# Optimization experiments

Hardware: AMD Instinct MI355X
Metric: run time of the kernel (lower is better)

Reference implementation:

```python
import jax, jax.numpy as jnp
import numpy as np

SIGMA_V = 0.1   # std of topic-level Gaussian noise theta_V
SCALE_R = 0.1   # 'sigma2_R' is used as the Normal scale in the torch code


def setup_inputs() -> dict:
    key = jax.random.key(0)
    ks = jax.random.split(key, 8)
    T, L, NT, KC, D = 20, 2000, 1000, 256, 5
    return {
        "Q": jax.random.normal(ks[0], (NT, 32), dtype=jnp.float32),
        "V": jax.random.normal(ks[1], (NT, KC), dtype=jnp.float32),
        "R": jax.random.uniform(ks[2], (T, L, NT), dtype=jnp.float32),
        "neighbor_weights": jax.random.normal(ks[3], (NT, NT), dtype=jnp.float32),
        "U": jax.random.normal(ks[4], (T, L, KC, D), dtype=jnp.float32),
        "U_emb_w": jax.random.normal(ks[5], (1, D), dtype=jnp.float32),
        "U_emb_b": jax.random.normal(ks[6], (1,), dtype=jnp.float32),
        "noise": jax.random.normal(ks[7], (NT, KC), dtype=jnp.float32),
        "C": jax.random.randint(jax.random.fold_in(key, 9), (T, L, NT), 0, 2, dtype=jnp.int32),
    }


def reference(Q, V, R, neighbor_weights, U, U_emb_w, U_emb_b, noise, C):
    # (nw[:, :, None] * V[None]).sum(0)[b, k] == V[b, k] * nw.sum(0)[b]
    # -> avoid materializing the (nt, nt, kc) intermediate.
    V_j = V * jnp.sum(neighbor_weights, axis=0)[:, None] + SIGMA_V * noise  # (nt, kc)
    # Linear(dim=5 -> 1) applied to U, then squeeze: (T, L, kc)
    U_emb = jnp.einsum('tlkd,d->tlk', U, U_emb_w[0]) + U_emb_b[0]
    # scores[t, i, j] = sigmoid(U_emb[t, i, :] . V_j[j, :])
    mu = jax.nn.sigmoid(jnp.einsum('tlk,jk->tlj', U_emb, V_j))  # (T, L, nt)
    # Normal(mu, SCALE_R).log_prob(R), summed over entries where C == 1
    log_prob = (-0.5 * jnp.square((R - mu) / SCALE_R)
                - jnp.log(SCALE_R) - 0.5 * jnp.log(2.0 * jnp.pi))
    return jnp.sum(jnp.where(C == 1, log_prob, 0.0))
```

## Files before the change

### kernel.cpp

```cpp
#include <hip/hip_runtime.h>
#include <hip/hip_bf16.h>

typedef __attribute__((ext_vector_type(8))) short short8;
typedef __attribute__((ext_vector_type(4))) float f32x4;
typedef __attribute__((ext_vector_type(4))) int   i32x4;

#define NTOP 1000
#define KC   256
#define MROWS 40000
#define MBLK  64

static __device__ __forceinline__ unsigned short f2bf(float x) {
    union { float f; unsigned u; } v; v.f = x;
    unsigned r = (v.u + 0x7FFFu + ((v.u >> 16) & 1u)) >> 16;
    return (unsigned short)r;
}

__global__ void k_prep(const float* __restrict__ nw,
                       float* __restrict__ colsum) {
    int j  = blockIdx.x * 256 + threadIdx.x;
    int i0 = blockIdx.y * 8;
    if (j < NTOP) {
        float s = 0.f;
        int iend = min(i0 + 8, NTOP);
        for (int i = i0; i < iend; ++i) s += nw[(size_t)i * NTOP + j];
        atomicAdd(colsum + j, s);
    }
}

__global__ void k_vj(const float* __restrict__ V,
                     const float* __restrict__ noise,
                     const float* __restrict__ colsum,
                     unsigned short* __restrict__ Bp) {
    int t  = blockIdx.x * 256 + threadIdx.x;
    int nt = t >> 9;
    int s  = (t >> 6) & 7;
    int l  = t & 63;
    int lm = l & 15, lq = l >> 4;
    int n  = nt * 16 + lm;
    int k0 = s * 32 + lq * 8;
    union { short8 v; unsigned short us[8]; } pk;
    if (n < NTOP) {
        float cs = colsum[n];
        #pragma unroll
        for (int j = 0; j < 8; ++j) {
            int idx = n * KC + k0 + j;
            pk.us[j] = f2bf(V[idx] * cs + 0.1f * noise[idx]);
        }
    } else {
        #pragma unroll
        for (int j = 0; j < 8; ++j) pk.us[j] = 0;
    }
    reinterpret_cast<short8*>(Bp)[t] = pk.v;
}

__global__ __launch_bounds__(256) void k_cmask(const int* __restrict__ C,
                                               unsigned* __restrict__ Cb) {
    const int idx = blockIdx.x * 256 + threadIdx.x;
    const int m = idx >> 5, w = idx & 31;
    const int* p = C + (size_t)m * NTOP + w * 32;
    const int nbase = w * 32;
    unsigned word = 0;
    if (nbase + 32 <= NTOP) {
        #pragma unroll
        for (int j = 0; j < 32; j += 4) {
            i32x4 c4 = *reinterpret_cast<const i32x4*>(p + j);
            word |= (unsigned)(c4.x == 1) << (j + 0);
            word |= (unsigned)(c4.y == 1) << (j + 1);
            word |= (unsigned)(c4.z == 1) << (j + 2);
            word |= (unsigned)(c4.w == 1) << (j + 3);
        }
    } else {
        for (int j = 0; j < NTOP - nbase; ++j)
            word |= (unsigned)(p[j] == 1) << j;
    }
    Cb[idx] = word;
}


#define SBAR __builtin_amdgcn_sched_barrier(0)

#define LOADBF8(nt_, B0,B1,B2,B3,B4,B5,B6,B7) do {                        \
    const short8* bp_ = Bf + ((((nt_) * 8) << 6) + l);                    \
    B0 = bp_[0*64]; B1 = bp_[1*64]; B2 = bp_[2*64]; B3 = bp_[3*64];       \
    B4 = bp_[4*64]; B5 = bp_[5*64]; B6 = bp_[6*64]; B7 = bp_[7*64];       \
} while (0)

#define LOADIT8(nt_, R0,R1,R2,R3, W0,W1,W2,W3) do {                       \
    const int nst_ = ((nt_) << 4) + (lq << 2);                            \
    if (nst_ < NTOP) {                                                    \
        const int ws_ = nst_ >> 5;                                        \
        R0 = *reinterpret_cast<const f32x4*>(R + rb0 + nst_);             \
        R1 = *reinterpret_cast<const f32x4*>(R + rb1 + nst_);             \
        R2 = *reinterpret_cast<const f32x4*>(R + rb2 + nst_);             \
        R3 = *reinterpret_cast<const f32x4*>(R + rb3 + nst_);             \
        W0 = Cb[cb0 + ws_]; W1 = Cb[cb1 + ws_];                           \
        W2 = Cb[cb2 + ws_]; W3 = Cb[cb3 + ws_];                           \
    } else {                                                              \
        R0 = (f32x4){0.f,0.f,0.f,0.f}; R1 = (f32x4){0.f,0.f,0.f,0.f};     \
        R2 = (f32x4){0.f,0.f,0.f,0.f}; R3 = (f32x4){0.f,0.f,0.f,0.f};     \
        W0 = 0u; W1 = 0u; W2 = 0u; W3 = 0u;                               \
    }                                                                     \
} while (0)

#define MF1(s_, B_) do {                                                  \
    const short8 a0_ = Afrag[0][s_][l];                                   \
    const short8 a1_ = Afrag[1][s_][l];                                   \
    const short8 a2_ = Afrag[2][s_][l];                                   \
    const short8 a3_ = Afrag[3][s_][l];                                   \
    acc0 = __builtin_amdgcn_mfma_f32_16x16x32_bf16(B_, a0_, acc0, 0,0,0); \
    acc1 = __builtin_amdgcn_mfma_f32_16x16x32_bf16(B_, a1_, acc1, 0,0,0); \
    acc2 = __builtin_amdgcn_mfma_f32_16x16x32_bf16(B_, a2_, acc2, 0,0,0); \
    acc3 = __builtin_amdgcn_mfma_f32_16x16x32_bf16(B_, a3_, acc3, 0,0,0); \
} while (0)

#define MFMA8(B0,B1,B2,B3,B4,B5,B6,B7) do {                               \
    acc0 = (f32x4){0.f,0.f,0.f,0.f}; acc1 = (f32x4){0.f,0.f,0.f,0.f};     \
    acc2 = (f32x4){0.f,0.f,0.f,0.f}; acc3 = (f32x4){0.f,0.f,0.f,0.f};     \
    MF1(0,B0); MF1(1,B1); MF1(2,B2); MF1(3,B3);                           \
    MF1(4,B4); MF1(5,B5); MF1(6,B6); MF1(7,B7);                           \
} while (0)

#define EPI1(ACC, RV, W_, SH) do {                                        \
    const unsigned y_ = (W_) >> (SH);                                     \
    _Pragma("unroll")                                                     \
    for (int r_ = 0; r_ < 4; ++r_) {                                      \
        float muv_ = 1.f / (1.f + __expf(-ACC[r_]));                      \
        float d_   = RV[r_] - muv_;                                       \
        float lp_  = -50.f * d_ * d_ + 1.3836465597893728f;               \
        if ((y_ >> r_) & 1u) lpsum += lp_;                                \
    }                                                                     \
} while (0)

#define EPI8(R0,R1,R2,R3, W0,W1,W2,W3, SH) do {                           \
    EPI1(acc0, R0, W0, SH); EPI1(acc1, R1, W1, SH);                       \
    EPI1(acc2, R2, W2, SH); EPI1(acc3, R3, W3, SH);                       \
} while (0)

__global__ __launch_bounds__(256, 2) void k_main(
    const float* __restrict__ U, const float* __restrict__ w5,
    const float* __restrict__ b1, const short8* __restrict__ Bf,
    const float* __restrict__ R, const unsigned* __restrict__ Cb,
    float* __restrict__ out)
{
    __shared__ short8 Afrag[4][8][64];
    __shared__ float  rawU[5120];

    const int tid  = threadIdx.x;
    const int wave = tid >> 6;
    const int l    = tid & 63;
    const int lm = l & 15;
    const int lq = l >> 4;
    const int m0 = blockIdx.x * MBLK;

    const float w0 = w5[0], w1 = w5[1], w2 = w5[2], w3 = w5[3], w4 = w5[4];
    const float bb = b1[0];

    const float* ub = U + (size_t)m0 * (KC * 5);
    for (int g = 0; g < 16; ++g) {
        const float* src = ub + (size_t)g * 5120;
        #pragma unroll
        for (int j = 0; j < 5; ++j) {
            const int idx = j * 1024 + tid * 4;
            *reinterpret_cast<f32x4*>(&rawU[idx]) =
                *reinterpret_cast<const f32x4*>(src + idx);
        }
        __syncthreads();
        if (tid < 128) {
            const int s   = tid >> 4;
            const int lqc = (tid >> 2) & 3;
            const int lmh = tid & 3;
            const int fi  = lmh * 1280 + s * 160 + lqc * 40;
            float u[40];
            #pragma unroll
            for (int i = 0; i < 10; ++i) {
                f32x4 t = *reinterpret_cast<const f32x4*>(&rawU[fi + i * 4]);
                u[i*4+0] = t.x; u[i*4+1] = t.y; u[i*4+2] = t.z; u[i*4+3] = t.w;
            }
            union { short8 v; unsigned short us[8]; } pk;
            #pragma unroll
            for (int j = 0; j < 8; ++j) {
                float e = u[j*5+0]*w0 + u[j*5+1]*w1 + u[j*5+2]*w2
                        + u[j*5+3]*w3 + u[j*5+4]*w4 + bb;
                pk.us[j] = f2bf(e);
            }
            const int mt = g >> 2;
            const int ll = lqc * 16 + ((g & 3) * 4 + lmh);
            Afrag[mt][s][ll] = pk.v;
        }
        __syncthreads();
    }

    const size_t rb0 = (size_t)(m0 +  0 + lm) * NTOP;
    const size_t rb1 = (size_t)(m0 + 16 + lm) * NTOP;
    const size_t rb2 = (size_t)(m0 + 32 + lm) * NTOP;
    const size_t rb3 = (size_t)(m0 + 48 + lm) * NTOP;
    const size_t cb0 = (size_t)(m0 +  0 + lm) * 32;
    const size_t cb1 = (size_t)(m0 + 16 + lm) * 32;
    const size_t cb2 = (size_t)(m0 + 32 + lm) * 32;
    const size_t cb3 = (size_t)(m0 + 48 + lm) * 32;

    float lpsum = 0.f;
    const int nt0 = wave << 4;
    const int shE = lq << 2;
    const int shO = 16 + (lq << 2);

    short8 pA0, pA1, pA2, pA3, pA4, pA5, pA6, pA7;
    short8 pB0, pB1, pB2, pB3, pB4, pB5, pB6, pB7;
    f32x4  rA0, rA1, rA2, rA3,  rB0, rB1, rB2, rB3;
    unsigned wA0, wA1, wA2, wA3,  wB0, wB1, wB2, wB3;
    f32x4  acc0, acc1, acc2, acc3;

    LOADBF8(nt0, pA0,pA1,pA2,pA3,pA4,pA5,pA6,pA7);
    LOADIT8(nt0, rA0,rA1,rA2,rA3, wA0,wA1,wA2,wA3);

    for (int it2 = 0; it2 < 8; ++it2) {
        const int ntE = nt0 + it2 * 2;

        SBAR;
        LOADBF8(ntE + 1, pB0,pB1,pB2,pB3,pB4,pB5,pB6,pB7);
        SBAR;
        MFMA8(pA0,pA1,pA2,pA3,pA4,pA5,pA6,pA7);
        SBAR;
        LOADIT8(ntE + 1, rB0,rB1,rB2,rB3, wB0,wB1,wB2,wB3);
        SBAR;
        EPI8(rA0,rA1,rA2,rA3, wA0,wA1,wA2,wA3, shE);

        SBAR;
        if (it2 < 7) { LOADBF8(ntE + 2, pA0,pA1,pA2,pA3,pA4,pA5,pA6,pA7); }
        SBAR;
        MFMA8(pB0,pB1,pB2,pB3,pB4,pB5,pB6,pB7);
        SBAR;
        if (it2 < 7) { LOADIT8(ntE + 2, rA0,rA1,rA2,rA3, wA0,wA1,wA2,wA3); }
        SBAR;
        EPI8(rB0,rB1,rB2,rB3, wB0,wB1,wB2,wB3, shO);
    }

    #pragma unroll
    for (int off = 32; off > 0; off >>= 1) lpsum += __shfl_down(lpsum, off);
    if (l == 0) atomicAdd(out, lpsum);
}

extern "C" void kernel_launch(void* const* d_in, const int* in_sizes, int n_in,
                              void* d_out, int out_size, void* d_ws, size_t ws_size,
                              hipStream_t stream) {
    const float* V     = (const float*)d_in[1];
    const float* R     = (const float*)d_in[2];
    const float* nw    = (const float*)d_in[3];
    const float* U     = (const float*)d_in[4];
    const float* w5    = (const float*)d_in[5];
    const float* b1    = (const float*)d_in[6];
    const float* noise = (const float*)d_in[7];
    const int*   C     = (const int*)d_in[8];
    float* out = (float*)d_out;

    float*          colsum = (float*)d_ws;
    unsigned short* Bp     = (unsigned short*)((char*)d_ws + 8192);
    unsigned*       Cb     = (unsigned*)((char*)d_ws + 532480);

    hipMemsetAsync(colsum, 0, NTOP * sizeof(float), stream);
    hipMemsetAsync(out, 0, sizeof(float), stream);
    hipLaunchKernelGGL(k_prep, dim3(4, 125), dim3(256), 0, stream, nw, colsum);
    hipLaunchKernelGGL(k_vj, dim3(128), dim3(256), 0, stream,
                       V, noise, colsum, Bp);
    hipLaunchKernelGGL(k_cmask, dim3(5000), dim3(256), 0, stream, C, Cb);
    hipLaunchKernelGGL(k_main, dim3(MROWS / MBLK), dim3(256), 0, stream,
                       U, w5, b1, (const short8*)Bp, R, Cb, out);
}
```

Baseline: 187.4 us.

## Prefetch U tiles in registers, pad LDS, and deepen main-loop prefetch

The U staging loop now keeps the next U chunk in registers while the current one is converted. The LDS rows are padded to 1284 floats to reduce bank conflicts. All 256 threads now share the bf16 embedding conversion, each doing half a fragment, where only 128 did before. The main loop prefetches two tiles ahead (A and B both loaded before the loop), and launch bounds ask for 3 blocks per SM. This adds register pressure, which may cause spills under the higher occupancy target.

```diff
diff --git a/kernel.cpp b/kernel.cpp
--- a/kernel.cpp
+++ b/kernel.cpp
@@ -4,6 +4,7 @@
 typedef __attribute__((ext_vector_type(8))) short short8;
 typedef __attribute__((ext_vector_type(4))) float f32x4;
 typedef __attribute__((ext_vector_type(4))) int   i32x4;
+typedef __attribute__((ext_vector_type(4))) unsigned short us4;
 
 #define NTOP 1000
 #define KC   256
@@ -137,14 +138,14 @@
     EPI1(acc2, R2, W2, SH); EPI1(acc3, R3, W3, SH);                       \
 } while (0)
 
-__global__ __launch_bounds__(256, 2) void k_main(
+__global__ __launch_bounds__(256, 3) void k_main(
     const float* __restrict__ U, const float* __restrict__ w5,
     const float* __restrict__ b1, const short8* __restrict__ Bf,
     const float* __restrict__ R, const unsigned* __restrict__ Cb,
     float* __restrict__ out)
 {
     __shared__ short8 Afrag[4][8][64];
-    __shared__ float  rawU[5120];
+    __shared__ float  rawU[4 * 1284];
 
     const int tid  = threadIdx.x;
     const int wave = tid >> 6;
@@ -156,39 +157,69 @@
     const float w0 = w5[0], w1 = w5[1], w2 = w5[2], w3 = w5[3], w4 = w5[4];
     const float bb = b1[0];
 
-    const float* ub = U + (size_t)m0 * (KC * 5);
-    for (int g = 0; g < 16; ++g) {
-        const float* src = ub + (size_t)g * 5120;
-        #pragma unroll
-        for (int j = 0; j < 5; ++j) {
-            const int idx = j * 1024 + tid * 4;
-            *reinterpret_cast<f32x4*>(&rawU[idx]) =
-                *reinterpret_cast<const f32x4*>(src + idx);
+    {
+        const float* ub = U + (size_t)m0 * (KC * 5);
+
+        float* dst0; float* dst1; float* dst2; float* dst3; float* dst4;
+        {
+            int i0 = 0 * 1024 + tid * 4; dst0 = &rawU[(i0 / 1280) * 1284 + i0 % 1280];
+            int i1 = 1 * 1024 + tid * 4; dst1 = &rawU[(i1 / 1280) * 1284 + i1 % 1280];
+            int i2 = 2 * 1024 + tid * 4; dst2 = &rawU[(i2 / 1280) * 1284 + i2 % 1280];
+            int i3 = 3 * 1024 + tid * 4; dst3 = &rawU[(i3 / 1280) * 1284 + i3 % 1280];
+            int i4 = 4 * 1024 + tid * 4; dst4 = &rawU[(i4 / 1280) * 1284 + i4 % 1280];
         }
-        __syncthreads();
-        if (tid < 128) {
-            const int s   = tid >> 4;
-            const int lqc = (tid >> 2) & 3;
-            const int lmh = tid & 3;
-            const int fi  = lmh * 1280 + s * 160 + lqc * 40;
-            float u[40];
-            #pragma unroll
-            for (int i = 0; i < 10; ++i) {
-                f32x4 t = *reinterpret_cast<const f32x4*>(&rawU[fi + i * 4]);
-                u[i*4+0] = t.x; u[i*4+1] = t.y; u[i*4+2] = t.z; u[i*4+3] = t.w;
+        const int chunk = tid >> 1;
+        const int half  = tid & 1;
+        const int s_c   = chunk >> 4;
+        const int lqc   = (chunk >> 2) & 3;
+        const int lmh   = chunk & 3;
+        const int fi    = lmh * 1284 + s_c * 160 + lqc * 40 + half * 20;
+
+        f32x4 st0, st1, st2, st3, st4;
+        st0 = *reinterpret_cast<const f32x4*>(ub + 0 * 1024 + tid * 4);
+        st1 = *reinterpret_cast<const f32x4*>(ub + 1 * 1024 + tid * 4);
+        st2 = *reinterpret_cast<const f32x4*>(ub + 2 * 1024 + tid * 4);
+        st3 = *reinterpret_cast<const f32x4*>(ub + 3 * 1024 + tid * 4);
+        st4 = *reinterpret_cast<const f32x4*>(ub + 4 * 1024 + tid * 4);
+
+        for (int g = 0; g < 16; ++g) {
+            *reinterpret_cast<f32x4*>(dst0) = st0;
+            *reinterpret_cast<f32x4*>(dst1) = st1;
+            *reinterpret_cast<f32x4*>(dst2) = st2;
+            *reinterpret_cast<f32x4*>(dst3) = st3;
+            *reinterpret_cast<f32x4*>(dst4) = st4;
+            __syncthreads();
+
+            if (g < 15) {
+                const float* src = ub + (size_t)(g + 1) * 5120;
+                st0 = *reinterpret_cast<const f32x4*>(src + 0 * 1024 + tid * 4);
+                st1 = *reinterpret_cast<const f32x4*>(src + 1 * 1024 + tid * 4);
+                st2 = *reinterpret_cast<const f32x4*>(src + 2 * 1024 + tid * 4);
+                st3 = *reinterpret_cast<const f32x4*>(src + 3 * 1024 + tid * 4);
+                st4 = *reinterpret_cast<const f32x4*>(src + 4 * 1024 + tid * 4);
             }
-            union { short8 v; unsigned short us[8]; } pk;
-            #pragma unroll
-            for (int j = 0; j < 8; ++j) {
-                float e = u[j*5+0]*w0 + u[j*5+1]*w1 + u[j*5+2]*w2
-                        + u[j*5+3]*w3 + u[j*5+4]*w4 + bb;
-                pk.us[j] = f2bf(e);
+
+            {
+                float u[20];
+                #pragma unroll
+                for (int i = 0; i < 5; ++i) {
+                    f32x4 t = *reinterpret_cast<const f32x4*>(&rawU[fi + i * 4]);
+                    u[i*4+0] = t.x; u[i*4+1] = t.y; u[i*4+2] = t.z; u[i*4+3] = t.w;
+                }
+                us4 pk;
+                #pragma unroll
+                for (int j = 0; j < 4; ++j) {
+                    float e = u[j*5+0]*w0 + u[j*5+1]*w1 + u[j*5+2]*w2
+                            + u[j*5+3]*w3 + u[j*5+4]*w4 + bb;
+                    pk[j] = f2bf(e);
+                }
+                const int mt = g >> 2;
+                const int ll = lqc * 16 + ((g & 3) * 4 + lmh);
+                *reinterpret_cast<us4*>(
+                    reinterpret_cast<unsigned short*>(&Afrag[mt][s_c][ll]) + half * 4) = pk;
             }
-            const int mt = g >> 2;
-            const int ll = lqc * 16 + ((g & 3) * 4 + lmh);
-            Afrag[mt][s][ll] = pk.v;
+            __syncthreads();
         }
-        __syncthreads();
     }
 
     const size_t rb0 = (size_t)(m0 +  0 + lm) * NTOP;
@@ -211,29 +242,31 @@
     unsigned wA0, wA1, wA2, wA3,  wB0, wB1, wB2, wB3;
     f32x4  acc0, acc1, acc2, acc3;
 
-    LOADBF8(nt0, pA0,pA1,pA2,pA3,pA4,pA5,pA6,pA7);
-    LOADIT8(nt0, rA0,rA1,rA2,rA3, wA0,wA1,wA2,wA3);
+    LOADBF8(nt0,     pA0,pA1,pA2,pA3,pA4,pA5,pA6,pA7);
+    LOADIT8(nt0,     rA0,rA1,rA2,rA3, wA0,wA1,wA2,wA3);
+    LOADBF8(nt0 + 1, pB0,pB1,pB2,pB3,pB4,pB5,pB6,pB7);
+    LOADIT8(nt0 + 1, rB0,rB1,rB2,rB3, wB0,wB1,wB2,wB3);
 
     for (int it2 = 0; it2 < 8; ++it2) {
         const int ntE = nt0 + it2 * 2;
 
-        SBAR;
-        LOADBF8(ntE + 1, pB0,pB1,pB2,pB3,pB4,pB5,pB6,pB7);
-        SBAR;
         MFMA8(pA0,pA1,pA2,pA3,pA4,pA5,pA6,pA7);
         SBAR;
-        LOADIT8(ntE + 1, rB0,rB1,rB2,rB3, wB0,wB1,wB2,wB3);
+        if (it2 < 7) { LOADBF8(ntE + 2, pA0,pA1,pA2,pA3,pA4,pA5,pA6,pA7); }
         SBAR;
         EPI8(rA0,rA1,rA2,rA3, wA0,wA1,wA2,wA3, shE);
-
-        SBAR;
-        if (it2 < 7) { LOADBF8(ntE + 2, pA0,pA1,pA2,pA3,pA4,pA5,pA6,pA7); }
-        SBAR;
+        SBAR;
+        if (it2 < 7) { LOADIT8(ntE + 2, rA0,rA1,rA2,rA3, wA0,wA1,wA2,wA3); }
+        SBAR;
+
         MFMA8(pB0,pB1,pB2,pB3,pB4,pB5,pB6,pB7);
         SBAR;
-        if (it2 < 7) { LOADIT8(ntE + 2, rA0,rA1,rA2,rA3, wA0,wA1,wA2,wA3); }
+        if (it2 < 7) { LOADBF8(ntE + 3, pB0,pB1,pB2,pB3,pB4,pB5,pB6,pB7); }
         SBAR;
         EPI8(rB0,rB1,rB2,rB3, wB0,wB1,wB2,wB3, shO);
+        SBAR;
+        if (it2 < 7) { LOADIT8(ntE + 3, rB0,rB1,rB2,rB3, wB0,wB1,wB2,wB3); }
+        SBAR;
     }
 
     #pragma unroll
```

After: 178.1 us. 1.05x faster.
